# Kernel optimization log

Measured on AMD Instinct MI355X. Metric: run time of the kernel, lower is better.

The kernel has to match this reference:

```python
import jax, jax.numpy as jnp
import numpy as np

IMG = 64            # image_height = image_width = 64
NPTS = 300          # n_pts_per_ray
MIN_DEPTH, MAX_DEPTH = 0.1, 3.0
GRID = 16           # latent_dim -> 16^3 voxel grid
VOXEL_SIZE = 0.1
FOV_DEG = 60.0      # pytorch3d FoVPerspectiveCameras default
B = 8               # number of cameras / latents
EPS = 1e-10         # EmissionAbsorptionRaymarcher eps


def _look_at(eye, at):
    # pytorch3d look_at_view_transform: row-vector convention x_view = x_world @ R + T
    up = np.array([0.0, 1.0, 0.0])
    z = at - eye; z = z / np.linalg.norm(z)
    x = np.cross(up, z); x = x / np.linalg.norm(x)
    y = np.cross(z, x); y = y / np.linalg.norm(y)
    R = np.stack([x, y, z], axis=1)  # columns are camera axes
    T = -eye @ R
    return R, T


def setup_inputs():
    rng = np.random.default_rng(0)
    Rs, Ts = [], []
    for _ in range(B):
        eye = rng.standard_normal(3) * np.array([0.01, 0.0001, 0.01])
        at = rng.standard_normal(3) * 0.01
        R, T = _look_at(eye, at)
        Rs.append(R); Ts.append(T)

    def lin(fan_in, fan_out):
        bound = 1.0 / np.sqrt(fan_in)  # torch Linear default init
        W = rng.uniform(-bound, bound, size=(fan_in, fan_out))
        b = rng.uniform(-bound, bound, size=(fan_out,))
        return jnp.asarray(W, jnp.float32), jnp.asarray(b, jnp.float32)

    W1, b1 = lin(30, 60)
    W2, b2 = lin(60, 480)
    W3, b3 = lin(480, 4 * GRID ** 3)
    zs = jnp.asarray(rng.standard_normal((B, 30)), jnp.float32)
    return {"zs": zs, "W1": W1, "b1": b1, "W2": W2, "b2": b2, "W3": W3, "b3": b3,
            "R": jnp.asarray(np.stack(Rs), jnp.float32),
            "T": jnp.asarray(np.stack(Ts), jnp.float32)}


def _grid_sample3d(vol, xyz):
    # vol: (C, D, H, W); xyz: (..., 3) in [-1, 1]; trilinear, align_corners=True, zero padding
    C, D, H, W = vol.shape
    batch_shape = xyz.shape[:-1]
    p = xyz.reshape(-1, 3)
    ix = (p[:, 0] + 1.0) * 0.5 * (W - 1)
    iy = (p[:, 1] + 1.0) * 0.5 * (H - 1)
    iz = (p[:, 2] + 1.0) * 0.5 * (D - 1)
    x0 = jnp.floor(ix); y0 = jnp.floor(iy); z0 = jnp.floor(iz)
    tx = ix - x0; ty = iy - y0; tz = iz - z0
    out = jnp.zeros((C, p.shape[0]), vol.dtype)
    for dx, wx in ((0, 1.0 - tx), (1, tx)):
        for dy, wy in ((0, 1.0 - ty), (1, ty)):
            for dz, wz in ((0, 1.0 - tz), (1, tz)):
                xf, yf, zf = x0 + dx, y0 + dy, z0 + dz
                valid = ((xf >= 0) & (xf <= W - 1) & (yf >= 0) & (yf <= H - 1)
                         & (zf >= 0) & (zf <= D - 1))
                xi = jnp.clip(xf, 0, W - 1).astype(jnp.int32)
                yi = jnp.clip(yf, 0, H - 1).astype(jnp.int32)
                zi = jnp.clip(zf, 0, D - 1).astype(jnp.int32)
                w = jnp.where(valid, wx * wy * wz, 0.0)
                out = out + w[None, :] * vol[:, zi, yi, xi]
    return jnp.moveaxis(out.reshape((C,) + batch_shape), 0, -1)


def _forward(zs, W1, b1, W2, b2, W3, b3, R, T):
    # latent MLP -> (B, 4, 16, 16, 16) volume (1 density channel + 3 color channels)
    h = jax.nn.sigmoid(zs @ W1 + b1)
    h = jax.nn.sigmoid(h @ W2 + b2)
    lat = jax.nn.sigmoid(h @ W3 + b3).reshape(-1, 4, GRID, GRID, GRID)
    densities = lat[:, 0:1]   # (B,1,D,H,W)
    colors = lat[:, 1:4]      # (B,3,D,H,W)

    # NDCGridRaysampler pixel-center grid (pytorch3d NDC: +x left, +y up, row 0 at max y)
    half_pix = 1.0 / IMG
    xs = jnp.linspace(1.0 - half_pix, -1.0 + half_pix, IMG)
    ys = jnp.linspace(1.0 - half_pix, -1.0 + half_pix, IMG)
    f = 1.0 / jnp.tan(jnp.deg2rad(FOV_DEG) / 2.0)  # focal from fov, aspect=1
    dir_cam = jnp.stack([jnp.broadcast_to(xs[None, :] / f, (IMG, IMG)),
                         jnp.broadcast_to(ys[:, None] / f, (IMG, IMG)),
                         jnp.ones((IMG, IMG))], axis=-1)  # (H,W,3)
    Rt = jnp.swapaxes(R, 1, 2)                             # view->world rotation
    dirs_w = jnp.einsum('hwc,bcd->bhwd', dir_cam, Rt)      # (B,H,W,3)
    origins_w = jnp.einsum('bc,bcd->bd', -T, Rt)           # camera centers (B,3)

    depths = jnp.linspace(MIN_DEPTH, MAX_DEPTH, NPTS)
    pts = origins_w[:, None, None, None, :] + dirs_w[:, :, :, None, :] * depths[None, None, None, :, None]
    half_extent = (GRID - 1) * VOXEL_SIZE * 0.5            # pytorch3d Volumes world->local scale
    local = pts / half_extent                              # (B,H,W,P,3)

    sigma = jax.vmap(_grid_sample3d)(densities, local)[..., 0]  # (B,H,W,P)
    feats = jax.vmap(_grid_sample3d)(colors, local)             # (B,H,W,P,3)

    # EmissionAbsorptionRaymarcher (surface_thickness=1)
    a = (1.0 + EPS) - sigma
    cp = jnp.cumprod(a, axis=-1)
    absorption = jnp.concatenate([jnp.ones_like(cp[..., :1]), cp[..., :-1]], axis=-1)
    weights = sigma * absorption
    rgb = jnp.sum(weights[..., None] * feats, axis=-2)          # (B,H,W,3)
    opacity = 1.0 - jnp.prod(1.0 - sigma, axis=-1, keepdims=True)
    return jnp.concatenate([rgb, opacity], axis=-1)             # (B,H,W,4)


def reference(zs, W1, b1, W2, b2, W3, b3, R, T):
    imgs = _forward(zs, W1, b1, W2, b2, W3, b3, R, T)
    return imgs[..., 3:4], imgs[..., 0:3]
```

## Files before the change

kernel.cpp:

```cpp
#include <hip/hip_runtime.h>
#include <hip/hip_bf16.h>

#define IMG 64
#define NPTS 300
#define GRIDN 16
#define BATCH 8

typedef __hip_bfloat16 bf16;

__device__ __forceinline__ float sigm(float x) { return 1.0f / (1.0f + __expf(-x)); }
__device__ __forceinline__ float lo_bf(unsigned u) { return __uint_as_float(u << 16); }
__device__ __forceinline__ float hi_bf(unsigned u) { return __uint_as_float(u & 0xffff0000u); }

template <typename T>
__device__ __forceinline__ float ldv(const void* p, int i);
template <>
__device__ __forceinline__ float ldv<float>(const void* p, int i) { return ((const float*)p)[i]; }
template <>
__device__ __forceinline__ float ldv<bf16>(const void* p, int i) {
    return __bfloat162float(((const bf16*)p)[i]);
}

__global__ void sniff_kernel(const void* w1, int* flag) {
    int t = threadIdx.x;
    float m = 0.0f;
    for (int i = t; i < 1800; i += 64) {
        float v = fabsf(__bfloat162float(((const bf16*)w1)[i]));
        if (!(v < 1e30f)) v = 1e30f;
        m = fmaxf(m, v);
    }
#pragma unroll
    for (int d = 1; d < 64; d <<= 1) m = fmaxf(m, __shfl_xor(m, d));
    if (t == 0) *flag = (m > 4.0f) ? 1 : 0;
}

template <typename T>
__device__ void mlp_h2_body(const void* zs, const void* W1, const void* b1, const void* W2,
                            const void* b2, float* __restrict__ h2) {
    int b = blockIdx.x, t = threadIdx.x;
    __shared__ float z[30];
    __shared__ float h1[60];
    if (t < 30) z[t] = ldv<T>(zs, b * 30 + t);
    __syncthreads();
    if (t < 60) {
        float acc = ldv<T>(b1, t);
        for (int i = 0; i < 30; ++i) acc += z[i] * ldv<T>(W1, i * 60 + t);
        h1[t] = sigm(acc);
    }
    __syncthreads();
    for (int j = t; j < 480; j += 64) {
        float acc = ldv<T>(b2, j);
        for (int i = 0; i < 60; ++i) acc += h1[i] * ldv<T>(W2, i * 480 + j);
        h2[b * 480 + j] = sigm(acc);
    }
}

__global__ void mlp_h2_kernel(const void* zs, const void* W1, const void* b1, const void* W2,
                              const void* b2, float* __restrict__ h2, const int* __restrict__ flag) {
    if (*flag)
        mlp_h2_body<float>(zs, W1, b1, W2, b2, h2);
    else
        mlp_h2_body<bf16>(zs, W1, b1, W2, b2, h2);
}

template <typename T>
__device__ void mlp_w3_body(const float* __restrict__ h2, const void* W3, const void* b3,
                            bf16* __restrict__ volbf) {
    __shared__ float h2s[BATCH * 480];
    int t = threadIdx.x;
    for (int i = t; i < BATCH * 480; i += 256) h2s[i] = h2[i];
    __syncthreads();
    int j = blockIdx.x * 256 + t;
    float bj = ldv<T>(b3, j);
    float acc[BATCH];
#pragma unroll
    for (int b = 0; b < BATCH; ++b) acc[b] = bj;
    for (int i = 0; i < 480; ++i) {
        float w = ldv<T>(W3, i * 16384 + j);
#pragma unroll
        for (int b = 0; b < BATCH; ++b) acc[b] = fmaf(h2s[b * 480 + i], w, acc[b]);
    }
    int c = j >> 12;
    int v = j & 4095;
#pragma unroll
    for (int b = 0; b < BATCH; ++b)
        volbf[(size_t)(b * 4096 + v) * 4 + c] = __float2bfloat16(sigm(acc[b]));
}

__global__ void mlp_w3_kernel(const float* __restrict__ h2, const void* W3, const void* b3,
                              bf16* __restrict__ volbf, const int* __restrict__ flag) {
    if (*flag)
        mlp_w3_body<float>(h2, W3, b3, volbf);
    else
        mlp_w3_body<bf16>(h2, W3, b3, volbf);
}

__global__ __launch_bounds__(256) void render_kernel(const void* Rm, const void* Tm,
                                                     const bf16* __restrict__ volbf, void* out,
                                                     const int* __restrict__ flag) {
    __shared__ uint2 vox[4096];
    int t = threadIdx.x;
    int rayBase = blockIdx.x * 64;
    int b = rayBase >> 12;
    const uint2* src = (const uint2*)(volbf + (size_t)b * 4096 * 4);
    for (int i = t; i < 4096; i += 256) vox[i] = src[i];
    __syncthreads();

    int f32out = *flag;
    int ray = rayBase + (t >> 2);
    int seg = t & 3;
    int pix = ray & 4095;
    int h = pix >> 6, w = pix & 63;

    const float inv_f = 0.57735026919f;
    float dcx = (0.984375f - 0.03125f * (float)w) * inv_f;
    float dcy = (0.984375f - 0.03125f * (float)h) * inv_f;

    float R[9], Tv[3];
    if (f32out) {
#pragma unroll
        for (int i = 0; i < 9; ++i) R[i] = ((const float*)Rm)[b * 9 + i];
#pragma unroll
        for (int i = 0; i < 3; ++i) Tv[i] = ((const float*)Tm)[b * 3 + i];
    } else {
#pragma unroll
        for (int i = 0; i < 9; ++i) R[i] = __bfloat162float(((const bf16*)Rm)[b * 9 + i]);
#pragma unroll
        for (int i = 0; i < 3; ++i) Tv[i] = __bfloat162float(((const bf16*)Tm)[b * 3 + i]);
    }

    float dx_ = dcx * R[0] + dcy * R[1] + R[2];
    float dy_ = dcx * R[3] + dcy * R[4] + R[5];
    float dz_ = dcx * R[6] + dcy * R[7] + R[8];
    float ox = -(Tv[0] * R[0] + Tv[1] * R[1] + Tv[2] * R[2]);
    float oy = -(Tv[0] * R[3] + Tv[1] * R[4] + Tv[2] * R[5]);
    float oz = -(Tv[0] * R[6] + Tv[1] * R[7] + Tv[2] * R[8]);

    float tA = -1e30f, tB = 1e30f;
    bool miss = false;
    {
        float dd[3] = {dx_, dy_, dz_}, oo[3] = {ox, oy, oz};
#pragma unroll
        for (int a = 0; a < 3; ++a) {
            if (fabsf(dd[a]) > 1e-8f) {
                float inv = 1.0f / dd[a];
                float ra = (-0.85f - oo[a]) * inv, rb = (0.85f - oo[a]) * inv;
                tA = fmaxf(tA, fminf(ra, rb));
                tB = fminf(tB, fmaxf(ra, rb));
            } else if (fabsf(oo[a]) >= 0.85f) {
                miss = true;
            }
        }
    }
    const float step = 2.9f / 299.0f;
    const float inv_step = 299.0f / 2.9f;
    int ilo = 0, ihi = -1;
    if (!miss && tB > tA) {
        float flo = fmaxf(-2.0f, fminf(302.0f, ceilf((tA - 0.1f) * inv_step)));
        float fhi = fmaxf(-2.0f, fminf(302.0f, floorf((tB - 0.1f) * inv_step)));
        ilo = (int)flo - 1;
        ihi = (int)fhi + 1;
        if (ilo < 0) ilo = 0;
        if (ihi > 299) ihi = 299;
    }
    int n = ihi - ilo + 1;
    if (n < 0) n = 0;
    int s0 = ilo + (n * seg) / 4;
    int s1 = ilo + (n * (seg + 1)) / 4;

    float cr = 0.f, cg = 0.f, cb = 0.f, Pa = 1.f, Po = 1.f;
    for (int i = s0; i < s1; ++i) {
        float tt = 0.1f + step * (float)i;
        float ix = fmaf(fmaf(tt, dx_, ox), 10.0f, 7.5f);
        float iy = fmaf(fmaf(tt, dy_, oy), 10.0f, 7.5f);
        float iz = fmaf(fmaf(tt, dz_, oz), 10.0f, 7.5f);
        float fx = floorf(ix), fy = floorf(iy), fz = floorf(iz);
        float txf = ix - fx, tyf = iy - fy, tzf = iz - fz;
        int x0 = (int)fx, y0 = (int)fy, z0 = (int)fz;
        float wx0 = (x0 >= 0 && x0 <= 15) ? (1.0f - txf) : 0.0f;
        float wx1 = (x0 >= -1 && x0 <= 14) ? txf : 0.0f;
        float wy0 = (y0 >= 0 && y0 <= 15) ? (1.0f - tyf) : 0.0f;
        float wy1 = (y0 >= -1 && y0 <= 14) ? tyf : 0.0f;
        float wz0 = (z0 >= 0 && z0 <= 15) ? (1.0f - tzf) : 0.0f;
        float wz1 = (z0 >= -1 && z0 <= 14) ? tzf : 0.0f;
        int xi0 = min(max(x0, 0), 15), xi1 = min(max(x0 + 1, 0), 15);
        int yi0 = min(max(y0, 0), 15), yi1 = min(max(y0 + 1, 0), 15);
        int zi0 = min(max(z0, 0), 15), zi1 = min(max(z0 + 1, 0), 15);

        float sx = 0.f, sr = 0.f, sg = 0.f, sb = 0.f;
#define CORN(W, ZI, YI, XI)                                 \
    {                                                       \
        uint2 q = vox[((ZI) << 8) + ((YI) << 4) + (XI)];    \
        sx = fmaf((W), lo_bf(q.x), sx);                     \
        sr = fmaf((W), hi_bf(q.x), sr);                     \
        sg = fmaf((W), lo_bf(q.y), sg);                     \
        sb = fmaf((W), hi_bf(q.y), sb);                     \
    }
        float wxy00 = wx0 * wy0, wxy10 = wx1 * wy0, wxy01 = wx0 * wy1, wxy11 = wx1 * wy1;
        CORN(wxy00 * wz0, zi0, yi0, xi0)
        CORN(wxy10 * wz0, zi0, yi0, xi1)
        CORN(wxy01 * wz0, zi0, yi1, xi0)
        CORN(wxy11 * wz0, zi0, yi1, xi1)
        CORN(wxy00 * wz1, zi1, yi0, xi0)
        CORN(wxy10 * wz1, zi1, yi0, xi1)
        CORN(wxy01 * wz1, zi1, yi1, xi0)
        CORN(wxy11 * wz1, zi1, yi1, xi1)
#undef CORN

        float wgt = sx * Pa;
        cr = fmaf(wgt, sr, cr);
        cg = fmaf(wgt, sg, cg);
        cb = fmaf(wgt, sb, cb);
        Pa *= (1.0f - sx);
        Po *= (1.0f - sx);
    }

#pragma unroll
    for (int d = 1; d < 4; d <<= 1) {
        float o_cr = __shfl_xor(cr, d);
        float o_cg = __shfl_xor(cg, d);
        float o_cb = __shfl_xor(cb, d);
        float o_Pa = __shfl_xor(Pa, d);
        float o_Po = __shfl_xor(Po, d);
        bool first = ((seg & d) == 0);
        cr = first ? fmaf(Pa, o_cr, cr) : fmaf(o_Pa, cr, o_cr);
        cg = first ? fmaf(Pa, o_cg, cg) : fmaf(o_Pa, cg, o_cg);
        cb = first ? fmaf(Pa, o_cb, cb) : fmaf(o_Pa, cb, o_cb);
        Pa *= o_Pa;
        Po *= o_Po;
    }

    if (seg == 0) {
        if (f32out) {
            float* of = (float*)out;
            of[ray] = 1.0f - Po;
            float* orgb = of + BATCH * IMG * IMG;
            orgb[ray * 3 + 0] = cr;
            orgb[ray * 3 + 1] = cg;
            orgb[ray * 3 + 2] = cb;
        } else {
            bf16* ob = (bf16*)out;
            ob[ray] = __float2bfloat16(1.0f - Po);
            bf16* orgb = ob + BATCH * IMG * IMG;
            orgb[ray * 3 + 0] = __float2bfloat16(cr);
            orgb[ray * 3 + 1] = __float2bfloat16(cg);
            orgb[ray * 3 + 2] = __float2bfloat16(cb);
        }
    }
}

extern "C" void kernel_launch(void* const* d_in, const int* in_sizes, int n_in,
                              void* d_out, int out_size, void* d_ws, size_t ws_size,
                              hipStream_t stream) {
    const void* zs = d_in[0];
    const void* W1 = d_in[1];
    const void* b1 = d_in[2];
    const void* W2 = d_in[3];
    const void* b2 = d_in[4];
    const void* W3 = d_in[5];
    const void* b3 = d_in[6];
    const void* Rm = d_in[7];
    const void* Tm = d_in[8];

    bf16* volbf = (bf16*)d_ws;
    float* h2 = (float*)((char*)d_ws + 262144);
    int* flag = (int*)((char*)d_ws + 277504);

    hipLaunchKernelGGL(sniff_kernel, dim3(1), dim3(64), 0, stream, W1, flag);
    hipLaunchKernelGGL(mlp_h2_kernel, dim3(BATCH), dim3(64), 0, stream, zs, W1, b1, W2, b2, h2, flag);
    hipLaunchKernelGGL(mlp_w3_kernel, dim3(64), dim3(256), 0, stream, h2, W3, b3, volbf, flag);
    hipLaunchKernelGGL(render_kernel, dim3(512), dim3(256), 0, stream, Rm, Tm, volbf, d_out, flag);
}
```

Before: 153.7 us.

## Split W3 layer into split-K partial and reduce kernels, fold sniff into MLP

The 480x16384 W3 matmul was done by only 64 blocks each looping over all 480 inputs. It is now split along K into 16 slices over a 16x16 grid with 4-wide vectorized weight loads, and a separate reduce kernel adds bias, applies the sigmoid and writes the bf16 volume. The dtype-sniff kernel is merged into the first MLP kernel to save a launch, and the redundant Po product in the renderer is dropped in favour of Pa. This adds an 8 MB partial buffer and an extra reduction pass, and falls back to the old path if the workspace is too small.

```diff
diff --git a/kernel.cpp b/kernel.cpp
--- a/kernel.cpp
+++ b/kernel.cpp
@@ -11,6 +11,9 @@
 __device__ __forceinline__ float sigm(float x) { return 1.0f / (1.0f + __expf(-x)); }
 __device__ __forceinline__ float lo_bf(unsigned u) { return __uint_as_float(u << 16); }
 __device__ __forceinline__ float hi_bf(unsigned u) { return __uint_as_float(u & 0xffff0000u); }
+__device__ __forceinline__ float us_bf(unsigned short u) {
+    return __uint_as_float(((unsigned)u) << 16);
+}
 
 template <typename T>
 __device__ __forceinline__ float ldv(const void* p, int i);
@@ -21,19 +24,6 @@
     return __bfloat162float(((const bf16*)p)[i]);
 }
 
-__global__ void sniff_kernel(const void* w1, int* flag) {
-    int t = threadIdx.x;
-    float m = 0.0f;
-    for (int i = t; i < 1800; i += 64) {
-        float v = fabsf(__bfloat162float(((const bf16*)w1)[i]));
-        if (!(v < 1e30f)) v = 1e30f;
-        m = fmaxf(m, v);
-    }
-#pragma unroll
-    for (int d = 1; d < 64; d <<= 1) m = fmaxf(m, __shfl_xor(m, d));
-    if (t == 0) *flag = (m > 4.0f) ? 1 : 0;
-}
-
 template <typename T>
 __device__ void mlp_h2_body(const void* zs, const void* W1, const void* b1, const void* W2,
                             const void* b2, float* __restrict__ h2) {
@@ -56,11 +46,91 @@
 }
 
 __global__ void mlp_h2_kernel(const void* zs, const void* W1, const void* b1, const void* W2,
-                              const void* b2, float* __restrict__ h2, const int* __restrict__ flag) {
-    if (*flag)
+                              const void* b2, float* __restrict__ h2, int* __restrict__ flag) {
+    int t = threadIdx.x;
+    float m = 0.0f;
+    for (int i = t; i < 1800; i += 64) {
+        float v = fabsf(__bfloat162float(((const bf16*)W1)[i]));
+        if (!(v < 1e30f)) v = 1e30f;
+        m = fmaxf(m, v);
+    }
+#pragma unroll
+    for (int d = 1; d < 64; d <<= 1) m = fmaxf(m, __shfl_xor(m, d));
+    int f = (m > 4.0f) ? 1 : 0;
+    if (blockIdx.x == 0 && t == 0) *flag = f;
+    if (f)
         mlp_h2_body<float>(zs, W1, b1, W2, b2, h2);
     else
         mlp_h2_body<bf16>(zs, W1, b1, W2, b2, h2);
+}
+
+template <typename T>
+__device__ void w3_partial_body(const float* __restrict__ h2, const void* W3,
+                                float* __restrict__ partial) {
+    __shared__ float h2s[BATCH][30];
+    int t = threadIdx.x;
+    int jb = blockIdx.x, s = blockIdx.y;
+    int i0 = s * 30;
+    if (t < 240) {
+        int b = t / 30, i = t - b * 30;
+        h2s[b][i] = h2[b * 480 + i0 + i];
+    }
+    __syncthreads();
+    int j0 = jb * 1024 + t * 4;
+    float acc[BATCH][4];
+#pragma unroll
+    for (int b = 0; b < BATCH; ++b)
+#pragma unroll
+        for (int c = 0; c < 4; ++c) acc[b][c] = 0.0f;
+
+#pragma unroll 6
+    for (int i = 0; i < 30; ++i) {
+        float w0, w1, w2, w3v;
+        if (sizeof(T) == 2) {
+            ushort4 q = *(const ushort4*)((const unsigned short*)W3 + (size_t)(i0 + i) * 16384 + j0);
+            w0 = us_bf(q.x); w1 = us_bf(q.y); w2 = us_bf(q.z); w3v = us_bf(q.w);
+        } else {
+            float4 q = *(const float4*)((const float*)W3 + (size_t)(i0 + i) * 16384 + j0);
+            w0 = q.x; w1 = q.y; w2 = q.z; w3v = q.w;
+        }
+#pragma unroll
+        for (int b = 0; b < BATCH; ++b) {
+            float h = h2s[b][i];
+            acc[b][0] = fmaf(h, w0, acc[b][0]);
+            acc[b][1] = fmaf(h, w1, acc[b][1]);
+            acc[b][2] = fmaf(h, w2, acc[b][2]);
+            acc[b][3] = fmaf(h, w3v, acc[b][3]);
+        }
+    }
+#pragma unroll
+    for (int b = 0; b < BATCH; ++b) {
+        float4 st = {acc[b][0], acc[b][1], acc[b][2], acc[b][3]};
+        *(float4*)(partial + ((size_t)(s * BATCH + b) << 14) + j0) = st;
+    }
+}
+
+__global__ __launch_bounds__(256) void w3_partial_kernel(const float* __restrict__ h2,
+                                                         const void* W3,
+                                                         float* __restrict__ partial,
+                                                         const int* __restrict__ flag) {
+    if (*flag)
+        w3_partial_body<float>(h2, W3, partial);
+    else
+        w3_partial_body<bf16>(h2, W3, partial);
+}
+
+__global__ __launch_bounds__(256) void w3_reduce_kernel(const float* __restrict__ partial,
+                                                        const void* b3, bf16* __restrict__ volbf,
+                                                        const int* __restrict__ flag) {
+    int tid = blockIdx.x * 256 + threadIdx.x;
+    int b = tid >> 14, j = tid & 16383;
+    float a = 0.0f;
+#pragma unroll
+    for (int s = 0; s < 16; ++s) a += partial[((size_t)(s * BATCH + b) << 14) + j];
+    a += (*flag) ? ldv<float>(b3, j) : ldv<bf16>(b3, j);
+    a = sigm(a);
+    int c = j >> 12, v = j & 4095;
+    volbf[(size_t)((b << 12) + v) * 4 + c] = __float2bfloat16(a);
 }
 
 template <typename T>
@@ -168,7 +238,7 @@
     int s0 = ilo + (n * seg) / 4;
     int s1 = ilo + (n * (seg + 1)) / 4;
 
-    float cr = 0.f, cg = 0.f, cb = 0.f, Pa = 1.f, Po = 1.f;
+    float cr = 0.f, cg = 0.f, cb = 0.f, Pa = 1.f;
     for (int i = s0; i < s1; ++i) {
         float tt = 0.1f + step * (float)i;
         float ix = fmaf(fmaf(tt, dx_, ox), 10.0f, 7.5f);
@@ -188,13 +258,13 @@
         int zi0 = min(max(z0, 0), 15), zi1 = min(max(z0 + 1, 0), 15);
 
         float sx = 0.f, sr = 0.f, sg = 0.f, sb = 0.f;
-#define CORN(W, ZI, YI, XI)                                 \
-    {                                                       \
-        uint2 q = vox[((ZI) << 8) + ((YI) << 4) + (XI)];    \
-        sx = fmaf((W), lo_bf(q.x), sx);                     \
-        sr = fmaf((W), hi_bf(q.x), sr);                     \
-        sg = fmaf((W), lo_bf(q.y), sg);                     \
-        sb = fmaf((W), hi_bf(q.y), sb);                     \
+#define CORN(W, ZI, YI, XI)                              \
+    {                                                    \
+        uint2 q = vox[((ZI) << 8) + ((YI) << 4) + (XI)]; \
+        sx = fmaf((W), lo_bf(q.x), sx);                  \
+        sr = fmaf((W), hi_bf(q.x), sr);                  \
+        sg = fmaf((W), lo_bf(q.y), sg);                  \
+        sb = fmaf((W), hi_bf(q.y), sb);                  \
     }
         float wxy00 = wx0 * wy0, wxy10 = wx1 * wy0, wxy01 = wx0 * wy1, wxy11 = wx1 * wy1;
         CORN(wxy00 * wz0, zi0, yi0, xi0)
@@ -212,7 +282,6 @@
         cg = fmaf(wgt, sg, cg);
         cb = fmaf(wgt, sb, cb);
         Pa *= (1.0f - sx);
-        Po *= (1.0f - sx);
     }
 
 #pragma unroll
@@ -221,26 +290,24 @@
         float o_cg = __shfl_xor(cg, d);
         float o_cb = __shfl_xor(cb, d);
         float o_Pa = __shfl_xor(Pa, d);
-        float o_Po = __shfl_xor(Po, d);
         bool first = ((seg & d) == 0);
         cr = first ? fmaf(Pa, o_cr, cr) : fmaf(o_Pa, cr, o_cr);
         cg = first ? fmaf(Pa, o_cg, cg) : fmaf(o_Pa, cg, o_cg);
         cb = first ? fmaf(Pa, o_cb, cb) : fmaf(o_Pa, cb, o_cb);
         Pa *= o_Pa;
-        Po *= o_Po;
     }
 
     if (seg == 0) {
         if (f32out) {
             float* of = (float*)out;
-            of[ray] = 1.0f - Po;
+            of[ray] = 1.0f - Pa;
             float* orgb = of + BATCH * IMG * IMG;
             orgb[ray * 3 + 0] = cr;
             orgb[ray * 3 + 1] = cg;
             orgb[ray * 3 + 2] = cb;
         } else {
             bf16* ob = (bf16*)out;
-            ob[ray] = __float2bfloat16(1.0f - Po);
+            ob[ray] = __float2bfloat16(1.0f - Pa);
             bf16* orgb = ob + BATCH * IMG * IMG;
             orgb[ray * 3 + 0] = __float2bfloat16(cr);
             orgb[ray * 3 + 1] = __float2bfloat16(cg);
@@ -262,12 +329,30 @@
     const void* Rm = d_in[7];
     const void* Tm = d_in[8];
 
+    const size_t PARTIAL_BYTES = (size_t)16 * BATCH * 16384 * 4;
+    const size_t NEED = 262144 + PARTIAL_BYTES + 15360 + 64;
+
     bf16* volbf = (bf16*)d_ws;
-    float* h2 = (float*)((char*)d_ws + 262144);
-    int* flag = (int*)((char*)d_ws + 277504);
-
-    hipLaunchKernelGGL(sniff_kernel, dim3(1), dim3(64), 0, stream, W1, flag);
-    hipLaunchKernelGGL(mlp_h2_kernel, dim3(BATCH), dim3(64), 0, stream, zs, W1, b1, W2, b2, h2, flag);
-    hipLaunchKernelGGL(mlp_w3_kernel, dim3(64), dim3(256), 0, stream, h2, W3, b3, volbf, flag);
-    hipLaunchKernelGGL(render_kernel, dim3(512), dim3(256), 0, stream, Rm, Tm, volbf, d_out, flag);
-}
+    if (ws_size >= NEED) {
+        float* partial = (float*)((char*)d_ws + 262144);
+        float* h2 = (float*)((char*)d_ws + 262144 + PARTIAL_BYTES);
+        int* flag = (int*)((char*)d_ws + 262144 + PARTIAL_BYTES + 15360);
+        hipLaunchKernelGGL(mlp_h2_kernel, dim3(BATCH), dim3(64), 0, stream, zs, W1, b1, W2, b2,
+                           h2, flag);
+        hipLaunchKernelGGL(w3_partial_kernel, dim3(16, 16), dim3(256), 0, stream, h2, W3,
+                           partial, flag);
+        hipLaunchKernelGGL(w3_reduce_kernel, dim3(512), dim3(256), 0, stream, partial, b3,
+                           volbf, flag);
+        hipLaunchKernelGGL(render_kernel, dim3(512), dim3(256), 0, stream, Rm, Tm, volbf, d_out,
+                           flag);
+    } else {
+        float* h2 = (float*)((char*)d_ws + 262144);
+        int* flag = (int*)((char*)d_ws + 277504);
+        hipLaunchKernelGGL(mlp_h2_kernel, dim3(BATCH), dim3(64), 0, stream, zs, W1, b1, W2, b2,
+                           h2, flag);
+        hipLaunchKernelGGL(mlp_w3_kernel, dim3(64), dim3(256), 0, stream, h2, W3, b3, volbf,
+                           flag);
+        hipLaunchKernelGGL(render_kernel, dim3(512), dim3(256), 0, stream, Rm, Tm, volbf, d_out,
+                           flag);
+    }
+}
```

Measured after the change: 130.0 us. 1.18x faster.

## Fuse MLP stages into split-K prep kernel and finalize volume inside render

Applied to the files above, without the earlier changes.

Replaces four launches (sniff, MLP layer 1-2, layer 3, render) with two. The prep kernel recomputes the small first two layers in every block and splits the large W3 product four ways along K across a 64x4 grid. The render kernel then sums the partials, adds the bias and applies the sigmoid while filling its shared voxel tile, and it redoes the dtype sniff itself. It also drops the duplicate Po product, since it always equals Pa. The aim is to cut launch overhead and get more parallelism out of the W3 GEMV, at the cost of redundant small-MLP and partial-reduction work in every block.

```diff
diff --git a/kernel.cpp b/kernel.cpp
--- a/kernel.cpp
+++ b/kernel.cpp
@@ -11,6 +11,14 @@
 __device__ __forceinline__ float sigm(float x) { return 1.0f / (1.0f + __expf(-x)); }
 __device__ __forceinline__ float lo_bf(unsigned u) { return __uint_as_float(u << 16); }
 __device__ __forceinline__ float hi_bf(unsigned u) { return __uint_as_float(u & 0xffff0000u); }
+__device__ __forceinline__ float us_bf(unsigned short u) {
+    return __uint_as_float(((unsigned)u) << 16);
+}
+__device__ __forceinline__ unsigned pack_bf2(float lo, float hi) {
+    bf16 l = __float2bfloat16(lo), h = __float2bfloat16(hi);
+    unsigned short ul = *(unsigned short*)&l, uh = *(unsigned short*)&h;
+    return (unsigned)ul | ((unsigned)uh << 16);
+}
 
 template <typename T>
 __device__ __forceinline__ float ldv(const void* p, int i);
@@ -21,92 +29,118 @@
     return __bfloat162float(((const bf16*)p)[i]);
 }
 
-__global__ void sniff_kernel(const void* w1, int* flag) {
+__device__ __forceinline__ void sniff(const void* W1, int* sflag, int t) {
+    if (t < 64) {
+        float m = 0.0f;
+        for (int i = t; i < 1800; i += 64) {
+            float v = fabsf(__bfloat162float(((const bf16*)W1)[i]));
+            if (!(v < 1e30f)) v = 1e30f;
+            m = fmaxf(m, v);
+        }
+#pragma unroll
+        for (int d = 1; d < 64; d <<= 1) m = fmaxf(m, __shfl_xor(m, d));
+        if (t == 0) *sflag = (m > 4.0f) ? 1 : 0;
+    }
+}
+
+template <typename T>
+__device__ void prep_body(const void* zs, const void* W1, const void* b1, const void* W2,
+                          const void* b2, const void* W3, float* __restrict__ partial) {
+    __shared__ float z[BATCH][30];
+    __shared__ float h1[BATCH][60];
+    __shared__ float h2s[BATCH][120];
     int t = threadIdx.x;
-    float m = 0.0f;
-    for (int i = t; i < 1800; i += 64) {
-        float v = fabsf(__bfloat162float(((const bf16*)w1)[i]));
-        if (!(v < 1e30f)) v = 1e30f;
-        m = fmaxf(m, v);
-    }
-#pragma unroll
-    for (int d = 1; d < 64; d <<= 1) m = fmaxf(m, __shfl_xor(m, d));
-    if (t == 0) *flag = (m > 4.0f) ? 1 : 0;
-}
-
-template <typename T>
-__device__ void mlp_h2_body(const void* zs, const void* W1, const void* b1, const void* W2,
-                            const void* b2, float* __restrict__ h2) {
-    int b = blockIdx.x, t = threadIdx.x;
-    __shared__ float z[30];
-    __shared__ float h1[60];
-    if (t < 30) z[t] = ldv<T>(zs, b * 30 + t);
-    __syncthreads();
-    if (t < 60) {
-        float acc = ldv<T>(b1, t);
-        for (int i = 0; i < 30; ++i) acc += z[i] * ldv<T>(W1, i * 60 + t);
-        h1[t] = sigm(acc);
-    }
-    __syncthreads();
-    for (int j = t; j < 480; j += 64) {
-        float acc = ldv<T>(b2, j);
-        for (int i = 0; i < 60; ++i) acc += h1[i] * ldv<T>(W2, i * 480 + j);
-        h2[b * 480 + j] = sigm(acc);
-    }
-}
-
-__global__ void mlp_h2_kernel(const void* zs, const void* W1, const void* b1, const void* W2,
-                              const void* b2, float* __restrict__ h2, const int* __restrict__ flag) {
-    if (*flag)
-        mlp_h2_body<float>(zs, W1, b1, W2, b2, h2);
+    int jb = blockIdx.x;
+    int ks = blockIdx.y;
+    int base = ks * 120;
+
+    if (t < 240) {
+        int b = t / 30, i = t - b * 30;
+        z[b][i] = ldv<T>(zs, t);
+    }
+    __syncthreads();
+    for (int idx = t; idx < 480; idx += 256) {
+        int b = idx / 60, j = idx - b * 60;
+        float acc = ldv<T>(b1, j);
+#pragma unroll
+        for (int i = 0; i < 30; ++i) acc = fmaf(z[b][i], ldv<T>(W1, i * 60 + j), acc);
+        h1[b][j] = sigm(acc);
+    }
+    __syncthreads();
+    for (int idx = t; idx < 960; idx += 256) {
+        int b = idx / 120, rr = idx - b * 120;
+        int col = base + rr;
+        float acc = ldv<T>(b2, col);
+#pragma unroll
+        for (int i = 0; i < 60; ++i) acc = fmaf(h1[b][i], ldv<T>(W2, i * 480 + col), acc);
+        h2s[b][rr] = sigm(acc);
+    }
+    __syncthreads();
+
+    int col = jb * 256 + t;
+    float acc[BATCH];
+#pragma unroll
+    for (int b = 0; b < BATCH; ++b) acc[b] = 0.0f;
+#pragma unroll 15
+    for (int r = 0; r < 120; ++r) {
+        int i = base + r;
+        float w;
+        if (sizeof(T) == 2)
+            w = us_bf(((const unsigned short*)W3)[(size_t)i * 16384 + col]);
+        else
+            w = ((const float*)W3)[(size_t)i * 16384 + col];
+#pragma unroll
+        for (int b = 0; b < BATCH; ++b) acc[b] = fmaf(h2s[b][r], w, acc[b]);
+    }
+#pragma unroll
+    for (int b = 0; b < BATCH; ++b)
+        partial[(((size_t)ks * BATCH + b) << 14) + col] = acc[b];
+}
+
+__global__ __launch_bounds__(256) void prep_kernel(const void* zs, const void* W1,
+                                                   const void* b1, const void* W2,
+                                                   const void* b2, const void* W3,
+                                                   float* __restrict__ partial) {
+    __shared__ int sflag;
+    int t = threadIdx.x;
+    sniff(W1, &sflag, t);
+    __syncthreads();
+    if (sflag)
+        prep_body<float>(zs, W1, b1, W2, b2, W3, partial);
     else
-        mlp_h2_body<bf16>(zs, W1, b1, W2, b2, h2);
-}
-
-template <typename T>
-__device__ void mlp_w3_body(const float* __restrict__ h2, const void* W3, const void* b3,
-                            bf16* __restrict__ volbf) {
-    __shared__ float h2s[BATCH * 480];
+        prep_body<bf16>(zs, W1, b1, W2, b2, W3, partial);
+}
+
+__global__ __launch_bounds__(256) void render_kernel(const void* W1, const void* b3,
+                                                     const void* Rm, const void* Tm,
+                                                     const float* __restrict__ partial,
+                                                     void* out) {
+    __shared__ uint2 vox[4096];
+    __shared__ int sflag;
     int t = threadIdx.x;
-    for (int i = t; i < BATCH * 480; i += 256) h2s[i] = h2[i];
-    __syncthreads();
-    int j = blockIdx.x * 256 + t;
-    float bj = ldv<T>(b3, j);
-    float acc[BATCH];
-#pragma unroll
-    for (int b = 0; b < BATCH; ++b) acc[b] = bj;
-    for (int i = 0; i < 480; ++i) {
-        float w = ldv<T>(W3, i * 16384 + j);
-#pragma unroll
-        for (int b = 0; b < BATCH; ++b) acc[b] = fmaf(h2s[b * 480 + i], w, acc[b]);
-    }
-    int c = j >> 12;
-    int v = j & 4095;
-#pragma unroll
-    for (int b = 0; b < BATCH; ++b)
-        volbf[(size_t)(b * 4096 + v) * 4 + c] = __float2bfloat16(sigm(acc[b]));
-}
-
-__global__ void mlp_w3_kernel(const float* __restrict__ h2, const void* W3, const void* b3,
-                              bf16* __restrict__ volbf, const int* __restrict__ flag) {
-    if (*flag)
-        mlp_w3_body<float>(h2, W3, b3, volbf);
-    else
-        mlp_w3_body<bf16>(h2, W3, b3, volbf);
-}
-
-__global__ __launch_bounds__(256) void render_kernel(const void* Rm, const void* Tm,
-                                                     const bf16* __restrict__ volbf, void* out,
-                                                     const int* __restrict__ flag) {
-    __shared__ uint2 vox[4096];
-    int t = threadIdx.x;
+    sniff(W1, &sflag, t);
+    __syncthreads();
+    int f32in = sflag;
+
     int rayBase = blockIdx.x * 64;
     int b = rayBase >> 12;
-    const uint2* src = (const uint2*)(volbf + (size_t)b * 4096 * 4);
-    for (int i = t; i < 4096; i += 256) vox[i] = src[i];
-    __syncthreads();
-
-    int f32out = *flag;
+
+    for (int r = 0; r < 16; ++r) {
+        int v = r * 256 + t;
+        float s[4];
+#pragma unroll
+        for (int c = 0; c < 4; ++c) {
+            int j = (c << 12) + v;
+            float a = f32in ? ((const float*)b3)[j] : us_bf(((const unsigned short*)b3)[j]);
+#pragma unroll
+            for (int ks = 0; ks < 4; ++ks)
+                a += partial[(((size_t)ks * BATCH + b) << 14) + j];
+            s[c] = sigm(a);
+        }
+        vox[v] = make_uint2(pack_bf2(s[0], s[1]), pack_bf2(s[2], s[3]));
+    }
+    __syncthreads();
+
     int ray = rayBase + (t >> 2);
     int seg = t & 3;
     int pix = ray & 4095;
@@ -117,7 +151,7 @@
     float dcy = (0.984375f - 0.03125f * (float)h) * inv_f;
 
     float R[9], Tv[3];
-    if (f32out) {
+    if (f32in) {
 #pragma unroll
         for (int i = 0; i < 9; ++i) R[i] = ((const float*)Rm)[b * 9 + i];
 #pragma unroll
@@ -168,7 +202,7 @@
     int s0 = ilo + (n * seg) / 4;
     int s1 = ilo + (n * (seg + 1)) / 4;
 
-    float cr = 0.f, cg = 0.f, cb = 0.f, Pa = 1.f, Po = 1.f;
+    float cr = 0.f, cg = 0.f, cb = 0.f, Pa = 1.f;
     for (int i = s0; i < s1; ++i) {
         float tt = 0.1f + step * (float)i;
         float ix = fmaf(fmaf(tt, dx_, ox), 10.0f, 7.5f);
@@ -188,13 +222,13 @@
         int zi0 = min(max(z0, 0), 15), zi1 = min(max(z0 + 1, 0), 15);
 
         float sx = 0.f, sr = 0.f, sg = 0.f, sb = 0.f;
-#define CORN(W, ZI, YI, XI)                                 \
-    {                                                       \
-        uint2 q = vox[((ZI) << 8) + ((YI) << 4) + (XI)];    \
-        sx = fmaf((W), lo_bf(q.x), sx);                     \
-        sr = fmaf((W), hi_bf(q.x), sr);                     \
-        sg = fmaf((W), lo_bf(q.y), sg);                     \
-        sb = fmaf((W), hi_bf(q.y), sb);                     \
+#define CORN(W, ZI, YI, XI)                              \
+    {                                                    \
+        uint2 q = vox[((ZI) << 8) + ((YI) << 4) + (XI)]; \
+        sx = fmaf((W), lo_bf(q.x), sx);                  \
+        sr = fmaf((W), hi_bf(q.x), sr);                  \
+        sg = fmaf((W), lo_bf(q.y), sg);                  \
+        sb = fmaf((W), hi_bf(q.y), sb);                  \
     }
         float wxy00 = wx0 * wy0, wxy10 = wx1 * wy0, wxy01 = wx0 * wy1, wxy11 = wx1 * wy1;
         CORN(wxy00 * wz0, zi0, yi0, xi0)
@@ -212,7 +246,6 @@
         cg = fmaf(wgt, sg, cg);
         cb = fmaf(wgt, sb, cb);
         Pa *= (1.0f - sx);
-        Po *= (1.0f - sx);
     }
 
 #pragma unroll
@@ -221,26 +254,24 @@
         float o_cg = __shfl_xor(cg, d);
         float o_cb = __shfl_xor(cb, d);
         float o_Pa = __shfl_xor(Pa, d);
-        float o_Po = __shfl_xor(Po, d);
         bool first = ((seg & d) == 0);
         cr = first ? fmaf(Pa, o_cr, cr) : fmaf(o_Pa, cr, o_cr);
         cg = first ? fmaf(Pa, o_cg, cg) : fmaf(o_Pa, cg, o_cg);
         cb = first ? fmaf(Pa, o_cb, cb) : fmaf(o_Pa, cb, o_cb);
         Pa *= o_Pa;
-        Po *= o_Po;
     }
 
     if (seg == 0) {
-        if (f32out) {
+        if (f32in) {
             float* of = (float*)out;
-            of[ray] = 1.0f - Po;
+            of[ray] = 1.0f - Pa;
             float* orgb = of + BATCH * IMG * IMG;
             orgb[ray * 3 + 0] = cr;
             orgb[ray * 3 + 1] = cg;
             orgb[ray * 3 + 2] = cb;
         } else {
             bf16* ob = (bf16*)out;
-            ob[ray] = __float2bfloat16(1.0f - Po);
+            ob[ray] = __float2bfloat16(1.0f - Pa);
             bf16* orgb = ob + BATCH * IMG * IMG;
             orgb[ray * 3 + 0] = __float2bfloat16(cr);
             orgb[ray * 3 + 1] = __float2bfloat16(cg);
@@ -262,12 +293,10 @@
     const void* Rm = d_in[7];
     const void* Tm = d_in[8];
 
-    bf16* volbf = (bf16*)d_ws;
-    float* h2 = (float*)((char*)d_ws + 262144);
-    int* flag = (int*)((char*)d_ws + 277504);
-
-    hipLaunchKernelGGL(sniff_kernel, dim3(1), dim3(64), 0, stream, W1, flag);
-    hipLaunchKernelGGL(mlp_h2_kernel, dim3(BATCH), dim3(64), 0, stream, zs, W1, b1, W2, b2, h2, flag);
-    hipLaunchKernelGGL(mlp_w3_kernel, dim3(64), dim3(256), 0, stream, h2, W3, b3, volbf, flag);
-    hipLaunchKernelGGL(render_kernel, dim3(512), dim3(256), 0, stream, Rm, Tm, volbf, d_out, flag);
-}
+    float* partial = (float*)d_ws;
+
+    hipLaunchKernelGGL(prep_kernel, dim3(64, 4), dim3(256), 0, stream, zs, W1, b1, W2, b2, W3,
+                       partial);
+    hipLaunchKernelGGL(render_kernel, dim3(512), dim3(256), 0, stream, W1, b3, Rm, Tm, partial,
+                       d_out);
+}
```

Measured after the change: 143.0 us. 7.0% less time.
